# Performance work log

Hardware: AMD Instinct MI355X
Metric: run time of the kernel (lower is better)

## Reference

```python
import jax, jax.numpy as jnp
from jax import lax
import numpy as np

EPS = 1e-6
DN = ('NCHW', 'OIHW', 'NCHW')  # conv dimension numbers matching torch F.conv2d


def setup_inputs() -> dict:
    key = jax.random.key(0)
    kx, ky = jax.random.split(key)
    B, C, H, W = 16, 3, 512, 512
    x = jax.random.normal(kx, (B, C, H, W), dtype=jnp.float32)
    y = jax.random.normal(ky, (B, C, H, W), dtype=jnp.float32)
    return {"x": x, "y": y}


def _box_smooth(v):
    # 7x7 uniform kernel repeated over 3 input channels -> 1 output channel,
    # every tap weighted 1/49 (matches kernel.repeat(1,3,1,1) in torch).
    k = jnp.full((1, v.shape[1], 7, 7), 1.0 / 49.0, dtype=v.dtype)
    return lax.conv_general_dilated(v, k, window_strides=(1, 1),
                                    padding=[(3, 3), (3, 3)],
                                    dimension_numbers=DN)


def reference(x, y):
    # conv is linear, so conv(x) - conv(y) == conv(x - y); avoids one conv pass
    diff = _box_smooth(x - y)           # [B, 1, H, W]
    return jnp.mean(jnp.sqrt(diff * diff + EPS))  # scalar Charbonnier loss
```

## Files before the change

### kernel.cpp

```cpp
#include <hip/hip_runtime.h>
#include <math.h>


namespace {
constexpr int kB = 16, kC = 3, kH = 512, kW = 512;
constexpr int TH = 32;
constexpr int TW = 64;
constexpr int RH = TH + 6;
constexpr int RW = TW + 8;
constexpr int RW4 = RW / 4;
constexpr int SLOTS = RH * RW4;
constexpr int NTHREADS = 256;
constexpr int K = 3;
}

__global__ __launch_bounds__(NTHREADS, 4)
void charbox_kernel(const float* __restrict__ x, const float* __restrict__ y,
                    float* __restrict__ out) {
  __shared__ float zs[RH][RW];
  __shared__ float red[NTHREADS / 64];

  const int tid = threadIdx.x;
  const int w0 = blockIdx.x * TW;
  const int h0 = blockIdx.y * TH;
  const int b  = blockIdx.z;

  const size_t HW = (size_t)kH * kW;
  const float* xb = x + (size_t)b * kC * HW;
  const float* yb = y + (size_t)b * kC * HW;
  const int cs4 = (int)(HW / 4);

  float4 xr[K][3], yr[K][3];
  const float4* xp[K];
  const float4* yp[K];
  bool img[K], ex[K];
  int  slot[K];
#pragma unroll
  for (int k = 0; k < K; ++k) {
    const int s  = tid + k * NTHREADS;
    const int r  = s / RW4;
    const int j4 = s - r * RW4;
    const int h  = h0 - 3 + r;
    const int wb = w0 - 4 + j4 * 4;
    slot[k] = s;
    ex[k]  = (s < SLOTS);
    img[k] = ex[k] & ((unsigned)h < (unsigned)kH) & ((unsigned)wb < (unsigned)kW);
    const long long o = (long long)h * kW + wb;
    xp[k] = (const float4*)(xb + o);
    yp[k] = (const float4*)(yb + o);
  }
#pragma unroll
  for (int k = 0; k < K; ++k) {
    if (img[k]) {
      xr[k][0] = xp[k][0]; xr[k][1] = xp[k][cs4]; xr[k][2] = xp[k][2 * cs4];
      yr[k][0] = yp[k][0]; yr[k][1] = yp[k][cs4]; yr[k][2] = yp[k][2 * cs4];
    }
  }
#pragma unroll
  for (int k = 0; k < K; ++k) {
    float4 z = make_float4(0.f, 0.f, 0.f, 0.f);
    if (img[k]) {
      z.x = (xr[k][0].x - yr[k][0].x) + (xr[k][1].x - yr[k][1].x) + (xr[k][2].x - yr[k][2].x);
      z.y = (xr[k][0].y - yr[k][0].y) + (xr[k][1].y - yr[k][1].y) + (xr[k][2].y - yr[k][2].y);
      z.z = (xr[k][0].z - yr[k][0].z) + (xr[k][1].z - yr[k][1].z) + (xr[k][2].z - yr[k][2].z);
      z.w = (xr[k][0].w - yr[k][0].w) + (xr[k][1].w - yr[k][1].w) + (xr[k][2].w - yr[k][2].w);
    }
    if (ex[k]) *(float4*)&((float*)zs)[slot[k] * 4] = z;
  }
  __syncthreads();

  const int wi = tid & 63;
  const int g  = tid >> 6;
  const int r0 = g * 8;

  float h[7];
  float v = 0.f;
#pragma unroll
  for (int k = 0; k < 7; ++k) {
    const float* zr = &zs[r0 + k][wi + 1];
    const float a = ((zr[0] + zr[1]) + (zr[2] + zr[3])) +
                    ((zr[4] + zr[5]) + zr[6]);
    h[k] = a;
    v += a;
  }
  float acc;
  {
    const float d = v * (1.0f / 49.0f);
    acc = sqrtf(fmaf(d, d, 1e-6f));
  }
#pragma unroll
  for (int k = 0; k < 7; ++k) {
    const float* zr = &zs[r0 + 7 + k][wi + 1];
    const float hn = ((zr[0] + zr[1]) + (zr[2] + zr[3])) +
                     ((zr[4] + zr[5]) + zr[6]);
    v += hn - h[k];
    const float d = v * (1.0f / 49.0f);
    acc += sqrtf(fmaf(d, d, 1e-6f));
  }

#pragma unroll
  for (int off = 32; off > 0; off >>= 1) acc += __shfl_down(acc, off, 64);
  if ((tid & 63) == 0) red[g] = acc;
  __syncthreads();
  if (tid == 0) {
    const float ssum = red[0] + red[1] + red[2] + red[3];
    atomicAdd(out, ssum * (1.0f / ((float)kB * (float)kH * (float)kW)));
  }
}

extern "C" void kernel_launch(void* const* d_in, const int* in_sizes, int n_in,
                              void* d_out, int out_size, void* d_ws, size_t ws_size,
                              hipStream_t stream) {
  const float* x = (const float*)d_in[0];
  const float* y = (const float*)d_in[1];
  float* out = (float*)d_out;

  dim3 grid(kW / TW, kH / TH, kB);
  charbox_kernel<<<grid, NTHREADS, 0, stream>>>(x, y, out);
}
```

Before: 130.8 us.

## Use persistent blocks with register prefetch of the next tile's loads

Replaces the one-tile-per-block grid with 512 persistent blocks, each looping over several tiles. Each iteration issues the global loads for the next tile into registers while the current tile's box filter runs from shared memory. Clamped addresses make the loads unconditional. The goal is to hide global memory latency and cut per-block launch and atomic overhead, at the cost of more live registers, an extra barrier per tile, and fewer blocks in flight.

```diff
diff --git a/kernel.cpp b/kernel.cpp
--- a/kernel.cpp
+++ b/kernel.cpp
@@ -10,97 +10,110 @@
 constexpr int RW = TW + 8;
 constexpr int RW4 = RW / 4;
 constexpr int SLOTS = RH * RW4;
-constexpr int NTHREADS = 256;
+constexpr int NT = 256;
 constexpr int K = 3;
+constexpr int NTILES = (kW / TW) * (kH / TH) * kB;
+constexpr int NBLOCKS = 512;
+constexpr int TPB = NTILES / NBLOCKS;
 }
 
-__global__ __launch_bounds__(NTHREADS, 4)
+__global__ __launch_bounds__(NT, 4)
 void charbox_kernel(const float* __restrict__ x, const float* __restrict__ y,
                     float* __restrict__ out) {
   __shared__ float zs[RH][RW];
-  __shared__ float red[NTHREADS / 64];
+  __shared__ float red[NT / 64];
 
   const int tid = threadIdx.x;
-  const int w0 = blockIdx.x * TW;
-  const int h0 = blockIdx.y * TH;
-  const int b  = blockIdx.z;
+  const size_t HW = (size_t)kH * kW;
 
-  const size_t HW = (size_t)kH * kW;
-  const float* xb = x + (size_t)b * kC * HW;
-  const float* yb = y + (size_t)b * kC * HW;
-  const int cs4 = (int)(HW / 4);
+  int rr[K], cc[K];
+  bool ex[K];
+#pragma unroll
+  for (int k = 0; k < K; ++k) {
+    const int s = tid + k * NT;
+    rr[k] = s / RW4;
+    cc[k] = (s - rr[k] * RW4) * 4;
+    ex[k] = (s < SLOTS);
+  }
 
   float4 xr[K][3], yr[K][3];
-  const float4* xp[K];
-  const float4* yp[K];
-  bool img[K], ex[K];
-  int  slot[K];
+  bool img[K];
+
+  auto issue = [&](int id) {
+    const int tx = id & 7, ty = (id >> 3) & 15, b = id >> 7;
+    const int w0 = tx * TW, h0 = ty * TH;
+    const float* xb = x + (size_t)b * kC * HW;
+    const float* yb = y + (size_t)b * kC * HW;
 #pragma unroll
-  for (int k = 0; k < K; ++k) {
-    const int s  = tid + k * NTHREADS;
-    const int r  = s / RW4;
-    const int j4 = s - r * RW4;
-    const int h  = h0 - 3 + r;
-    const int wb = w0 - 4 + j4 * 4;
-    slot[k] = s;
-    ex[k]  = (s < SLOTS);
-    img[k] = ex[k] & ((unsigned)h < (unsigned)kH) & ((unsigned)wb < (unsigned)kW);
-    const long long o = (long long)h * kW + wb;
-    xp[k] = (const float4*)(xb + o);
-    yp[k] = (const float4*)(yb + o);
-  }
-#pragma unroll
-  for (int k = 0; k < K; ++k) {
-    if (img[k]) {
-      xr[k][0] = xp[k][0]; xr[k][1] = xp[k][cs4]; xr[k][2] = xp[k][2 * cs4];
-      yr[k][0] = yp[k][0]; yr[k][1] = yp[k][cs4]; yr[k][2] = yp[k][2 * cs4];
+    for (int k = 0; k < K; ++k) {
+      const int h  = h0 - 3 + rr[k];
+      const int wb = w0 - 4 + cc[k];
+      img[k] = ex[k] & ((unsigned)h < (unsigned)kH) & ((unsigned)wb < (unsigned)kW);
+      const int hc = min(max(h, 0), kH - 1);
+      const int wc = min(max(wb, 0), kW - 4);
+      const float* px = xb + (size_t)hc * kW + wc;
+      const float* py = yb + (size_t)hc * kW + wc;
+      xr[k][0] = *(const float4*)px;
+      xr[k][1] = *(const float4*)(px + HW);
+      xr[k][2] = *(const float4*)(px + 2 * HW);
+      yr[k][0] = *(const float4*)py;
+      yr[k][1] = *(const float4*)(py + HW);
+      yr[k][2] = *(const float4*)(py + 2 * HW);
     }
-  }
-#pragma unroll
-  for (int k = 0; k < K; ++k) {
-    float4 z = make_float4(0.f, 0.f, 0.f, 0.f);
-    if (img[k]) {
-      z.x = (xr[k][0].x - yr[k][0].x) + (xr[k][1].x - yr[k][1].x) + (xr[k][2].x - yr[k][2].x);
-      z.y = (xr[k][0].y - yr[k][0].y) + (xr[k][1].y - yr[k][1].y) + (xr[k][2].y - yr[k][2].y);
-      z.z = (xr[k][0].z - yr[k][0].z) + (xr[k][1].z - yr[k][1].z) + (xr[k][2].z - yr[k][2].z);
-      z.w = (xr[k][0].w - yr[k][0].w) + (xr[k][1].w - yr[k][1].w) + (xr[k][2].w - yr[k][2].w);
-    }
-    if (ex[k]) *(float4*)&((float*)zs)[slot[k] * 4] = z;
-  }
-  __syncthreads();
+  };
 
+  float acc = 0.f;
   const int wi = tid & 63;
   const int g  = tid >> 6;
   const int r0 = g * 8;
 
-  float h[7];
-  float v = 0.f;
+  issue(blockIdx.x);
+
+  for (int it = 0; it < TPB; ++it) {
 #pragma unroll
-  for (int k = 0; k < 7; ++k) {
-    const float* zr = &zs[r0 + k][wi + 1];
-    const float a = ((zr[0] + zr[1]) + (zr[2] + zr[3])) +
-                    ((zr[4] + zr[5]) + zr[6]);
-    h[k] = a;
-    v += a;
-  }
-  float acc;
-  {
-    const float d = v * (1.0f / 49.0f);
-    acc = sqrtf(fmaf(d, d, 1e-6f));
-  }
+    for (int k = 0; k < K; ++k) {
+      if (ex[k]) {
+        float4 z = make_float4(0.f, 0.f, 0.f, 0.f);
+        if (img[k]) {
+          z.x = (xr[k][0].x - yr[k][0].x) + (xr[k][1].x - yr[k][1].x) + (xr[k][2].x - yr[k][2].x);
+          z.y = (xr[k][0].y - yr[k][0].y) + (xr[k][1].y - yr[k][1].y) + (xr[k][2].y - yr[k][2].y);
+          z.z = (xr[k][0].z - yr[k][0].z) + (xr[k][1].z - yr[k][1].z) + (xr[k][2].z - yr[k][2].z);
+          z.w = (xr[k][0].w - yr[k][0].w) + (xr[k][1].w - yr[k][1].w) + (xr[k][2].w - yr[k][2].w);
+        }
+        *(float4*)&zs[rr[k]][cc[k]] = z;
+      }
+    }
+    __syncthreads();
+
+    if (it + 1 < TPB) issue((it + 1) * NBLOCKS + blockIdx.x);
+
+    float hbuf[7];
+    float v = 0.f;
 #pragma unroll
-  for (int k = 0; k < 7; ++k) {
-    const float* zr = &zs[r0 + 7 + k][wi + 1];
-    const float hn = ((zr[0] + zr[1]) + (zr[2] + zr[3])) +
-                     ((zr[4] + zr[5]) + zr[6]);
-    v += hn - h[k];
-    const float d = v * (1.0f / 49.0f);
-    acc += sqrtf(fmaf(d, d, 1e-6f));
+    for (int k = 0; k < 7; ++k) {
+      const float* zr = &zs[r0 + k][wi + 1];
+      const float a = ((zr[0] + zr[1]) + (zr[2] + zr[3])) + ((zr[4] + zr[5]) + zr[6]);
+      hbuf[k] = a;
+      v += a;
+    }
+    {
+      const float d = v * (1.0f / 49.0f);
+      acc += sqrtf(fmaf(d, d, 1e-6f));
+    }
+#pragma unroll
+    for (int k = 0; k < 7; ++k) {
+      const float* zr = &zs[r0 + 7 + k][wi + 1];
+      const float hn = ((zr[0] + zr[1]) + (zr[2] + zr[3])) + ((zr[4] + zr[5]) + zr[6]);
+      v += hn - hbuf[k];
+      const float d = v * (1.0f / 49.0f);
+      acc += sqrtf(fmaf(d, d, 1e-6f));
+    }
+    __syncthreads();
   }
 
 #pragma unroll
   for (int off = 32; off > 0; off >>= 1) acc += __shfl_down(acc, off, 64);
-  if ((tid & 63) == 0) red[g] = acc;
+  if (wi == 0) red[g] = acc;
   __syncthreads();
   if (tid == 0) {
     const float ssum = red[0] + red[1] + red[2] + red[3];
@@ -115,6 +128,5 @@
   const float* y = (const float*)d_in[1];
   float* out = (float*)d_out;
 
-  dim3 grid(kW / TW, kH / TH, kB);
-  charbox_kernel<<<grid, NTHREADS, 0, stream>>>(x, y, out);
+  charbox_kernel<<<NBLOCKS, NT, 0, stream>>>(x, y, out);
 }
```

Result: faster. 122.0 us (-6.7%).
